# Kernel optimization log

Hardware: AMD Instinct MI355X
Metric: run time of the kernel (lower is better)

The kernel has to match this reference:

```python
import jax, jax.numpy as jnp
import numpy as np

D_MODEL = 256
N_HEADS = 8
D_HEAD = D_MODEL // N_HEADS
B = 65536
LN_EPS = 1e-5


def setup_inputs() -> dict:
    key = jax.random.key(0)
    ks = jax.random.split(key, 6)
    s = 1.0 / np.sqrt(D_MODEL)
    x = jax.random.normal(ks[0], (B, D_MODEL), dtype=jnp.float32)
    Wq = jax.random.normal(ks[1], (D_MODEL, D_MODEL), dtype=jnp.float32) * s
    Wk = jax.random.normal(ks[2], (D_MODEL, D_MODEL), dtype=jnp.float32) * s
    Wv = jax.random.normal(ks[3], (D_MODEL, D_MODEL), dtype=jnp.float32) * s
    Wout = jax.random.normal(ks[4], (D_MODEL, D_MODEL), dtype=jnp.float32) * s
    b_out = jnp.zeros((D_MODEL,), dtype=jnp.float32)
    # L initialized to identity per head (matches nn.init.eye_) plus tiny noise
    L = jnp.broadcast_to(jnp.eye(D_HEAD, dtype=jnp.float32), (N_HEADS, D_HEAD, D_HEAD)) \
        + 0.01 * jax.random.normal(ks[5], (N_HEADS, D_HEAD, D_HEAD), dtype=jnp.float32)
    gamma = jnp.ones((D_MODEL,), dtype=jnp.float32)
    beta = jnp.zeros((D_MODEL,), dtype=jnp.float32)
    return {"x": x, "Wq": Wq, "Wk": Wk, "Wv": Wv, "Wout": Wout,
            "b_out": b_out, "L": L, "gamma": gamma, "beta": beta}


def reference(x, Wq, Wk, Wv, Wout, b_out, L, gamma, beta):
    b = x.shape[0]
    # projections; view as [B, H, d_head]
    Q = (x @ Wq).reshape(b, N_HEADS, D_HEAD)
    K = (x @ Wk).reshape(b, N_HEADS, D_HEAD)
    V = (x @ Wv).reshape(b, N_HEADS, D_HEAD)
    # pairwise head differences: [B, Hq, Hk, d_head]
    diff = Q[:, :, None, :] - K[:, None, :, :]
    # per-key-head learned metric transform: L indexed by key head
    diff_t = jnp.einsum('bqkd,kdf->bqkf', diff, L)
    sq_dist = jnp.sum(diff_t * diff_t, axis=-1)            # [B, Hq, Hk]
    attn = jax.nn.softmax(-sq_dist / jnp.sqrt(jnp.float32(D_HEAD)), axis=2)
    out = jnp.einsum('bqk,bkd->bqd', attn, V).reshape(b, D_MODEL)
    out = out @ Wout + b_out
    h = out + x
    # LayerNorm over last dim
    mu = jnp.mean(h, axis=-1, keepdims=True)
    var = jnp.mean((h - mu) ** 2, axis=-1, keepdims=True)
    return (h - mu) * jax.lax.rsqrt(var + LN_EPS) * gamma + beta
```

## Files before the change

### kernel.cpp

```cpp
#include <hip/hip_runtime.h>


typedef __bf16 bf16x8 __attribute__((ext_vector_type(8)));
typedef _Float16 f16x8 __attribute__((ext_vector_type(8)));
typedef float  f32x4  __attribute__((ext_vector_type(4)));
typedef int    i32x4  __attribute__((ext_vector_type(4)));
typedef int    i32x2  __attribute__((ext_vector_type(2)));
typedef unsigned short u16;

__device__ __forceinline__ float bf2f(u16 u){
  unsigned int x = ((unsigned int)u) << 16;
  return __builtin_bit_cast(float, x);
}
__device__ __forceinline__ u16 f2bf(float f){
  unsigned int u = __builtin_bit_cast(unsigned int, f);
  u += 0x7FFFu + ((u >> 16) & 1u);
  return (u16)(u >> 16);
}
__device__ __forceinline__ unsigned int pk2(float lo, float hi){
  return ((unsigned int)f2bf(hi) << 16) | (unsigned int)f2bf(lo);
}
__device__ __forceinline__ bf16x8 ldfrag(const u16* p){
  return __builtin_bit_cast(bf16x8, *(const i32x4*)p);
}

#define LROW 264

__global__ __launch_bounds__(256) void geo_prep(
    const float* __restrict__ Wq, const float* __restrict__ Wk,
    const float* __restrict__ Wv, const float* __restrict__ Wout,
    const float* __restrict__ L, u16* __restrict__ ws)
{
  u16* Wd    = ws;
  u16* WvT   = ws + 524288;
  u16* WoutT = ws + 589824;
  const int b = blockIdx.x, t = threadIdx.x;

  if (b < 64){
    const int q = b >> 3, k = b & 7;
    __shared__ float dwb[256][33];
    __shared__ float Lk[32][33];
    for (int i = 0; i < 4; ++i){
      int idx = t + i*256;
      Lk[idx >> 5][idx & 31] = L[k*1024 + idx];
    }
    {
      const int c = t;
      const float* wqp = Wq + c*256 + q*32;
      const float* wkp = Wk + c*256 + k*32;
      #pragma unroll
      for (int j = 0; j < 8; ++j){
        f32x4 a  = *(const f32x4*)(wqp + j*4);
        f32x4 bb = *(const f32x4*)(wkp + j*4);
        #pragma unroll
        for (int p = 0; p < 4; ++p) dwb[c][j*4 + p] = a[p] - bb[p];
      }
    }
    __syncthreads();
    const int c = t;
    float wreg[32];
    #pragma unroll
    for (int d = 0; d < 32; ++d) wreg[d] = dwb[c][d];
    for (int f = 0; f < 32; ++f){
      float s = 0.f;
      #pragma unroll
      for (int d = 0; d < 32; ++d) s = fmaf(wreg[d], Lk[d][f], s);
      Wd[(size_t)(q*256 + k*32 + f)*256 + c] = f2bf(s);
    }
  } else {
    const int bb  = b - 64;
    const float* src = (bb < 16) ? Wv  : Wout;
    u16*         dst = (bb < 16) ? WvT : WoutT;
    const int tile = bb & 15;
    const int tr = tile >> 2, tc = tile & 3;
    __shared__ float tlf[64][68];
    {
      const int row = t >> 2, cs = (t & 3)*16;
      #pragma unroll
      for (int j = 0; j < 4; ++j){
        f32x4 v = *(const f32x4*)(src + (size_t)(tr*64 + row)*256 + tc*64 + cs + j*4);
        #pragma unroll
        for (int p = 0; p < 4; ++p) tlf[row][cs + j*4 + p] = v[p];
      }
    }
    __syncthreads();
    {
      const int n = t >> 2, cs = (t & 3)*16;
      float us[16];
      #pragma unroll
      for (int j = 0; j < 16; ++j) us[j] = tlf[cs + j][n];
      #pragma unroll
      for (int h = 0; h < 2; ++h){
        i32x4 o;
        #pragma unroll
        for (int p = 0; p < 4; ++p)
          o[p] = (int)pk2(us[h*8 + 2*p], us[h*8 + 2*p + 1]);
        *(i32x4*)(dst + (size_t)(tc*64 + n)*256 + tr*64 + cs + h*8) = o;
      }
    }
  }
}

__global__ __launch_bounds__(512, 4) void geo_fused(
    const float* __restrict__ x,   const u16* __restrict__ Wd,
    const u16* __restrict__ WvT,   const u16* __restrict__ WoutT,
    const float* __restrict__ b_out, const float* __restrict__ gamma,
    const float* __restrict__ beta,  float* __restrict__ out)
{
  __shared__ __align__(16) char pool[75776];
  u16  (*xs)[LROW] = (u16 (*)[LROW])(pool);
  u16  (*Vs)[LROW] = (u16 (*)[LROW])(pool + 33792);
  u16  (*ao)[LROW] = (u16 (*)[LROW])(pool);
  u16  (*hs)[256]  = (u16 (*)[256])(pool + 33792);
  _Float16* sqh    = (_Float16*)(pool + 67584);

  const int t    = threadIdx.x;
  const int lane = t & 63;
  const int w    = t >> 6;
  const int l15  = lane & 15;
  const int quad = lane >> 4;
  const long rowbase = (long)blockIdx.x * 64;

  {
    const int r  = t >> 3;
    const int c0 = (t & 7) * 32;
    const float* src = x + (rowbase + r)*256 + c0;
    unsigned int words[16];
    #pragma unroll
    for (int j = 0; j < 8; ++j){
      f32x4 v = *(const f32x4*)(src + j*4);
      words[j*2    ] = pk2(v[0], v[1]);
      words[j*2 + 1] = pk2(v[2], v[3]);
    }
    #pragma unroll
    for (int qd = 0; qd < 4; ++qd){
      i32x4 o;
      #pragma unroll
      for (int p = 0; p < 4; ++p) o[p] = (int)words[qd*4 + p];
      *(i32x4*)&xs[r][c0 + qd*8] = o;
    }
  }
  __syncthreads();

  {
    f32x4 acc[4][2];
    #pragma unroll
    for (int mt = 0; mt < 4; ++mt)
      #pragma unroll
      for (int nt = 0; nt < 2; ++nt) acc[mt][nt] = f32x4{0.f,0.f,0.f,0.f};
    #pragma unroll
    for (int kk = 0; kk < 8; ++kk){
      const int c0 = kk*32 + quad*8;
      bf16x8 a[4], bfr[2];
      #pragma unroll
      for (int mt = 0; mt < 4; ++mt) a[mt] = ldfrag(&xs[mt*16 + l15][c0]);
      #pragma unroll
      for (int nt = 0; nt < 2; ++nt){
        const int n = w*32 + nt*16 + l15;
        bfr[nt] = __builtin_bit_cast(bf16x8, *(const i32x4*)(WvT + (size_t)n*256 + c0));
      }
      #pragma unroll
      for (int mt = 0; mt < 4; ++mt)
        #pragma unroll
        for (int nt = 0; nt < 2; ++nt)
          acc[mt][nt] = __builtin_amdgcn_mfma_f32_16x16x32_bf16(a[mt], bfr[nt], acc[mt][nt], 0, 0, 0);
    }
    #pragma unroll
    for (int mt = 0; mt < 4; ++mt)
      #pragma unroll
      for (int nt = 0; nt < 2; ++nt){
        const int col = w*32 + nt*16 + l15;
        #pragma unroll
        for (int reg = 0; reg < 4; ++reg)
          Vs[mt*16 + quad*4 + reg][col] = f2bf(acc[mt][nt][reg]);
      }
  }

  {
    #pragma unroll
    for (int kp = 0; kp < 4; ++kp){
      f32x4 acc[2][2][4];
      #pragma unroll
      for (int k2 = 0; k2 < 2; ++k2)
        #pragma unroll
        for (int mt = 0; mt < 2; ++mt)
          #pragma unroll
          for (int nt = 0; nt < 4; ++nt) acc[k2][mt][nt] = f32x4{0.f,0.f,0.f,0.f};
      #pragma unroll
      for (int kk = 0; kk < 8; ++kk){
        const int c0 = kk*32 + quad*8;
        bf16x8 bfr[4];
        #pragma unroll
        for (int nt = 0; nt < 4; ++nt) bfr[nt] = ldfrag(&xs[nt*16 + l15][c0]);
        bf16x8 a[2][2];
        #pragma unroll
        for (int k2 = 0; k2 < 2; ++k2)
          #pragma unroll
          for (int mt = 0; mt < 2; ++mt){
            const int m = w*256 + (kp*2 + k2)*32 + mt*16 + l15;
            a[k2][mt] = __builtin_bit_cast(bf16x8, *(const i32x4*)(Wd + (size_t)m*256 + c0));
          }
        #pragma unroll
        for (int k2 = 0; k2 < 2; ++k2)
          #pragma unroll
          for (int mt = 0; mt < 2; ++mt)
            #pragma unroll
            for (int nt = 0; nt < 4; ++nt)
              acc[k2][mt][nt] = __builtin_amdgcn_mfma_f32_16x16x32_bf16(a[k2][mt], bfr[nt], acc[k2][mt][nt], 0, 0, 0);
      }
      #pragma unroll
      for (int k2 = 0; k2 < 2; ++k2){
        const int k = kp*2 + k2;
        #pragma unroll
        for (int nt = 0; nt < 4; ++nt){
          float s = 0.f;
          #pragma unroll
          for (int mt = 0; mt < 2; ++mt)
            #pragma unroll
            for (int reg = 0; reg < 4; ++reg){
              float d = acc[k2][mt][nt][reg];
              s = fmaf(d, d, s);
            }
          s += __shfl_xor(s, 16);
          s += __shfl_xor(s, 32);
          if (quad == 0)
            sqh[w*512 + (nt*16 + l15)*8 + k] =
                (_Float16)(s * -0.17677669529663687f);
        }
      }
    }
  }
  __syncthreads();

  {
    #pragma unroll
    for (int nt = 0; nt < 4; ++nt){
      const int r = nt*16 + l15;
      f16x8 lgh = __builtin_bit_cast(f16x8, *(const i32x4*)&sqh[w*512 + r*8]);
      float lg[8];
      #pragma unroll
      for (int k = 0; k < 8; ++k) lg[k] = (float)lgh[k];
      float mx = lg[0];
      #pragma unroll
      for (int k = 1; k < 8; ++k) mx = fmaxf(mx, lg[k]);
      float e[8], sum = 0.f;
      #pragma unroll
      for (int k = 0; k < 8; ++k){ e[k] = __expf(lg[k] - mx); sum += e[k]; }
      const float inv = 1.0f / sum;
      float o[8] = {0.f,0.f,0.f,0.f,0.f,0.f,0.f,0.f};
      #pragma unroll
      for (int k = 0; k < 8; ++k){
        i32x4 v = *(const i32x4*)&Vs[r][k*32 + quad*8];
        const float a = e[k] * inv;
        #pragma unroll
        for (int p = 0; p < 4; ++p){
          unsigned int u = (unsigned int)v[p];
          o[2*p    ] = fmaf(a, __builtin_bit_cast(float, u << 16),          o[2*p    ]);
          o[2*p + 1] = fmaf(a, __builtin_bit_cast(float, u & 0xFFFF0000u),  o[2*p + 1]);
        }
      }
      i32x4 pkv;
      #pragma unroll
      for (int p = 0; p < 4; ++p) pkv[p] = (int)pk2(o[2*p], o[2*p + 1]);
      *(i32x4*)&ao[r][w*32 + quad*8] = pkv;
    }
  }
  __syncthreads();

  {
    f32x4 acc[4][2];
    #pragma unroll
    for (int mt = 0; mt < 4; ++mt)
      #pragma unroll
      for (int nt = 0; nt < 2; ++nt) acc[mt][nt] = f32x4{0.f,0.f,0.f,0.f};
    #pragma unroll
    for (int kk = 0; kk < 8; ++kk){
      const int c0 = kk*32 + quad*8;
      bf16x8 a[4], bfr[2];
      #pragma unroll
      for (int mt = 0; mt < 4; ++mt) a[mt] = ldfrag(&ao[mt*16 + l15][c0]);
      #pragma unroll
      for (int nt = 0; nt < 2; ++nt){
        const int n = w*32 + nt*16 + l15;
        bfr[nt] = __builtin_bit_cast(bf16x8, *(const i32x4*)(WoutT + (size_t)n*256 + c0));
      }
      #pragma unroll
      for (int mt = 0; mt < 4; ++mt)
        #pragma unroll
        for (int nt = 0; nt < 2; ++nt)
          acc[mt][nt] = __builtin_amdgcn_mfma_f32_16x16x32_bf16(a[mt], bfr[nt], acc[mt][nt], 0, 0, 0);
    }
    #pragma unroll
    for (int nt = 0; nt < 2; ++nt){
      const int col = w*32 + nt*16 + l15;
      const float bo = b_out[col];
      #pragma unroll
      for (int mt = 0; mt < 4; ++mt)
        #pragma unroll
        for (int reg = 0; reg < 4; ++reg){
          const int row = mt*16 + quad*4 + reg;
          hs[row][col] = f2bf(acc[mt][nt][reg] + bo);
        }
    }
  }
  __syncthreads();

  {
    #pragma unroll
    for (int rr = 0; rr < 8; ++rr){
      const int r = w*8 + rr;
      const int c = lane*4;
      i32x2 hv2 = *(const i32x2*)&hs[r][c];
      f32x4 xv  = *(const f32x4*)(x + (rowbase + r)*256 + c);
      unsigned int u0 = (unsigned int)hv2[0], u1 = (unsigned int)hv2[1];
      f32x4 hv;
      hv[0] = __builtin_bit_cast(float, u0 << 16)         + xv[0];
      hv[1] = __builtin_bit_cast(float, u0 & 0xFFFF0000u) + xv[1];
      hv[2] = __builtin_bit_cast(float, u1 << 16)         + xv[2];
      hv[3] = __builtin_bit_cast(float, u1 & 0xFFFF0000u) + xv[3];
      float s  = hv[0] + hv[1] + hv[2] + hv[3];
      float s2 = hv[0]*hv[0] + hv[1]*hv[1] + hv[2]*hv[2] + hv[3]*hv[3];
      #pragma unroll
      for (int off = 1; off < 64; off <<= 1){
        s  += __shfl_xor(s,  off);
        s2 += __shfl_xor(s2, off);
      }
      const float mu  = s  * (1.0f/256.0f);
      const float var = s2 * (1.0f/256.0f) - mu*mu;
      const float rs  = rsqrtf(var + 1e-5f);
      f32x4 gv = *(const f32x4*)(gamma + c);
      f32x4 bv = *(const f32x4*)(beta  + c);
      f32x4 y;
      y[0] = (hv[0] - mu)*rs*gv[0] + bv[0];
      y[1] = (hv[1] - mu)*rs*gv[1] + bv[1];
      y[2] = (hv[2] - mu)*rs*gv[2] + bv[2];
      y[3] = (hv[3] - mu)*rs*gv[3] + bv[3];
      *(f32x4*)(out + (rowbase + r)*256 + c) = y;
    }
  }
}

extern "C" void kernel_launch(void* const* d_in, const int* in_sizes, int n_in,
                              void* d_out, int out_size, void* d_ws, size_t ws_size,
                              hipStream_t stream)
{
  const float* x     = (const float*)d_in[0];
  const float* Wq    = (const float*)d_in[1];
  const float* Wk    = (const float*)d_in[2];
  const float* Wv    = (const float*)d_in[3];
  const float* Wout  = (const float*)d_in[4];
  const float* b_out = (const float*)d_in[5];
  const float* L     = (const float*)d_in[6];
  const float* gamma = (const float*)d_in[7];
  const float* beta  = (const float*)d_in[8];
  u16* ws = (u16*)d_ws;

  geo_prep<<<96, 256, 0, stream>>>(Wq, Wk, Wv, Wout, L, ws);
  geo_fused<<<1024, 512, 0, stream>>>(x, ws, ws + 524288, ws + 589824,
                                      b_out, gamma, beta, (float*)d_out);
}
```

Measured before the change: 307.3 us.

## Compute Q,K,V projections then apply per-head L via MFMA instead of pairwise Wd GEMM

Replaces the precomputed 2048x256 pairwise-difference weight (Wq-Wk)·L with separate Q/K/V projections. L is then applied with small per-head MFMAs to K once and to Q for each key head, and squared distances are formed as (QL - KL). This cuts the projection work from a 2048-wide GEMM to three 256-wide GEMMs. Rows per block are halved to 32, the grid is doubled, and LDS use shrinks. Forming differences after bf16 rounding of QL and KL may lose precision compared with projecting the difference directly.

```diff
diff --git a/kernel.cpp b/kernel.cpp
--- a/kernel.cpp
+++ b/kernel.cpp
@@ -2,7 +2,6 @@
 
 
 typedef __bf16 bf16x8 __attribute__((ext_vector_type(8)));
-typedef _Float16 f16x8 __attribute__((ext_vector_type(8)));
 typedef float  f32x4  __attribute__((ext_vector_type(4)));
 typedef int    i32x4  __attribute__((ext_vector_type(4)));
 typedef int    i32x2  __attribute__((ext_vector_type(2)));
@@ -20,7 +19,10 @@
 __device__ __forceinline__ unsigned int pk2(float lo, float hi){
   return ((unsigned int)f2bf(hi) << 16) | (unsigned int)f2bf(lo);
 }
-__device__ __forceinline__ bf16x8 ldfrag(const u16* p){
+__device__ __forceinline__ bf16x8 ldfrag_lds(const u16* p){
+  return __builtin_bit_cast(bf16x8, *(const i32x4*)p);
+}
+__device__ __forceinline__ bf16x8 ldfrag_g(const u16* p){
   return __builtin_bit_cast(bf16x8, *(const i32x4*)p);
 }
 
@@ -31,47 +33,12 @@
     const float* __restrict__ Wv, const float* __restrict__ Wout,
     const float* __restrict__ L, u16* __restrict__ ws)
 {
-  u16* Wd    = ws;
-  u16* WvT   = ws + 524288;
-  u16* WoutT = ws + 589824;
   const int b = blockIdx.x, t = threadIdx.x;
-
   if (b < 64){
-    const int q = b >> 3, k = b & 7;
-    __shared__ float dwb[256][33];
-    __shared__ float Lk[32][33];
-    for (int i = 0; i < 4; ++i){
-      int idx = t + i*256;
-      Lk[idx >> 5][idx & 31] = L[k*1024 + idx];
-    }
-    {
-      const int c = t;
-      const float* wqp = Wq + c*256 + q*32;
-      const float* wkp = Wk + c*256 + k*32;
-      #pragma unroll
-      for (int j = 0; j < 8; ++j){
-        f32x4 a  = *(const f32x4*)(wqp + j*4);
-        f32x4 bb = *(const f32x4*)(wkp + j*4);
-        #pragma unroll
-        for (int p = 0; p < 4; ++p) dwb[c][j*4 + p] = a[p] - bb[p];
-      }
-    }
-    __syncthreads();
-    const int c = t;
-    float wreg[32];
-    #pragma unroll
-    for (int d = 0; d < 32; ++d) wreg[d] = dwb[c][d];
-    for (int f = 0; f < 32; ++f){
-      float s = 0.f;
-      #pragma unroll
-      for (int d = 0; d < 32; ++d) s = fmaf(wreg[d], Lk[d][f], s);
-      Wd[(size_t)(q*256 + k*32 + f)*256 + c] = f2bf(s);
-    }
-  } else {
-    const int bb  = b - 64;
-    const float* src = (bb < 16) ? Wv  : Wout;
-    u16*         dst = (bb < 16) ? WvT : WoutT;
-    const int tile = bb & 15;
+    const int m = b >> 4;
+    const float* src = (m == 0) ? Wq : (m == 1) ? Wk : (m == 2) ? Wv : Wout;
+    u16* dstbase = (m < 3) ? (ws + m*65536) : (ws + 196608);
+    const int tile = b & 15;
     const int tr = tile >> 2, tc = tile & 3;
     __shared__ float tlf[64][68];
     {
@@ -95,224 +62,238 @@
         #pragma unroll
         for (int p = 0; p < 4; ++p)
           o[p] = (int)pk2(us[h*8 + 2*p], us[h*8 + 2*p + 1]);
-        *(i32x4*)(dst + (size_t)(tc*64 + n)*256 + tr*64 + cs + h*8) = o;
-      }
-    }
+        *(i32x4*)(dstbase + (size_t)(tc*64 + n)*256 + tr*64 + cs + h*8) = o;
+      }
+    }
+  } else {
+    u16* Lt = ws + 262144;
+    const int k = t >> 5, f = t & 31;
+    for (int d = 0; d < 32; ++d)
+      Lt[k*1024 + f*32 + d] = f2bf(L[k*1024 + d*32 + f]);
   }
 }
 
 __global__ __launch_bounds__(512, 4) void geo_fused(
-    const float* __restrict__ x,   const u16* __restrict__ Wd,
-    const u16* __restrict__ WvT,   const u16* __restrict__ WoutT,
+    const float* __restrict__ x,     const u16* __restrict__ WqkvT,
+    const u16* __restrict__ WoutT,   const u16* __restrict__ Lt,
     const float* __restrict__ b_out, const float* __restrict__ gamma,
     const float* __restrict__ beta,  float* __restrict__ out)
 {
-  __shared__ __align__(16) char pool[75776];
-  u16  (*xs)[LROW] = (u16 (*)[LROW])(pool);
-  u16  (*Vs)[LROW] = (u16 (*)[LROW])(pool + 33792);
-  u16  (*ao)[LROW] = (u16 (*)[LROW])(pool);
-  u16  (*hs)[256]  = (u16 (*)[256])(pool + 33792);
-  _Float16* sqh    = (_Float16*)(pool + 67584);
+  __shared__ __align__(16) char pool[67584];
+  u16* xsU  = (u16*)(pool);
+  u16* KtsU = (u16*)(pool);
+  u16* QsU  = (u16*)(pool + 16896);
+  u16* hsU  = (u16*)(pool + 16896);
+  u16* KsU  = (u16*)(pool + 33792);
+  u16* aoU  = (u16*)(pool + 33792);
+  u16* VsU  = (u16*)(pool + 50688);
 
   const int t    = threadIdx.x;
   const int lane = t & 63;
   const int w    = t >> 6;
   const int l15  = lane & 15;
   const int quad = lane >> 4;
-  const long rowbase = (long)blockIdx.x * 64;
-
-  {
-    const int r  = t >> 3;
-    const int c0 = (t & 7) * 32;
+  const long rowbase = (long)blockIdx.x * 32;
+
+  {
+    const int r  = t >> 4;
+    const int c0 = (t & 15) * 16;
     const float* src = x + (rowbase + r)*256 + c0;
-    unsigned int words[16];
-    #pragma unroll
-    for (int j = 0; j < 8; ++j){
+    unsigned int wds[8];
+    #pragma unroll
+    for (int j = 0; j < 4; ++j){
       f32x4 v = *(const f32x4*)(src + j*4);
-      words[j*2    ] = pk2(v[0], v[1]);
-      words[j*2 + 1] = pk2(v[2], v[3]);
-    }
-    #pragma unroll
-    for (int qd = 0; qd < 4; ++qd){
+      wds[j*2    ] = pk2(v[0], v[1]);
+      wds[j*2 + 1] = pk2(v[2], v[3]);
+    }
+    #pragma unroll
+    for (int h = 0; h < 2; ++h){
       i32x4 o;
       #pragma unroll
-      for (int p = 0; p < 4; ++p) o[p] = (int)words[qd*4 + p];
-      *(i32x4*)&xs[r][c0 + qd*8] = o;
-    }
-  }
-  __syncthreads();
-
-  {
-    f32x4 acc[4][2];
-    #pragma unroll
-    for (int mt = 0; mt < 4; ++mt)
+      for (int p = 0; p < 4; ++p) o[p] = (int)wds[h*4 + p];
+      *(i32x4*)&xsU[r*LROW + c0 + h*8] = o;
+    }
+  }
+  __syncthreads();
+
+  #pragma unroll
+  for (int s = 0; s < 3; ++s){
+    const u16* Bbase = WqkvT + (size_t)(s*256 + w*32)*256;
+    u16* dst = (s == 0) ? QsU : (s == 1) ? KsU : VsU;
+    f32x4 acc[2][2];
+    #pragma unroll
+    for (int mt = 0; mt < 2; ++mt)
       #pragma unroll
       for (int nt = 0; nt < 2; ++nt) acc[mt][nt] = f32x4{0.f,0.f,0.f,0.f};
     #pragma unroll
     for (int kk = 0; kk < 8; ++kk){
       const int c0 = kk*32 + quad*8;
-      bf16x8 a[4], bfr[2];
-      #pragma unroll
-      for (int mt = 0; mt < 4; ++mt) a[mt] = ldfrag(&xs[mt*16 + l15][c0]);
-      #pragma unroll
-      for (int nt = 0; nt < 2; ++nt){
-        const int n = w*32 + nt*16 + l15;
-        bfr[nt] = __builtin_bit_cast(bf16x8, *(const i32x4*)(WvT + (size_t)n*256 + c0));
-      }
-      #pragma unroll
-      for (int mt = 0; mt < 4; ++mt)
+      bf16x8 a[2], bb[2];
+      #pragma unroll
+      for (int mt = 0; mt < 2; ++mt) a[mt] = ldfrag_lds(&xsU[(mt*16 + l15)*LROW + c0]);
+      #pragma unroll
+      for (int nt = 0; nt < 2; ++nt) bb[nt] = ldfrag_g(Bbase + (size_t)(nt*16 + l15)*256 + c0);
+      #pragma unroll
+      for (int mt = 0; mt < 2; ++mt)
         #pragma unroll
         for (int nt = 0; nt < 2; ++nt)
-          acc[mt][nt] = __builtin_amdgcn_mfma_f32_16x16x32_bf16(a[mt], bfr[nt], acc[mt][nt], 0, 0, 0);
-    }
-    #pragma unroll
-    for (int mt = 0; mt < 4; ++mt)
+          acc[mt][nt] = __builtin_amdgcn_mfma_f32_16x16x32_bf16(a[mt], bb[nt], acc[mt][nt], 0, 0, 0);
+    }
+    #pragma unroll
+    for (int mt = 0; mt < 2; ++mt)
       #pragma unroll
       for (int nt = 0; nt < 2; ++nt){
         const int col = w*32 + nt*16 + l15;
         #pragma unroll
         for (int reg = 0; reg < 4; ++reg)
-          Vs[mt*16 + quad*4 + reg][col] = f2bf(acc[mt][nt][reg]);
-      }
-  }
-
-  {
-    #pragma unroll
-    for (int kp = 0; kp < 4; ++kp){
-      f32x4 acc[2][2][4];
-      #pragma unroll
-      for (int k2 = 0; k2 < 2; ++k2)
-        #pragma unroll
-        for (int mt = 0; mt < 2; ++mt)
-          #pragma unroll
-          for (int nt = 0; nt < 4; ++nt) acc[k2][mt][nt] = f32x4{0.f,0.f,0.f,0.f};
-      #pragma unroll
-      for (int kk = 0; kk < 8; ++kk){
-        const int c0 = kk*32 + quad*8;
-        bf16x8 bfr[4];
-        #pragma unroll
-        for (int nt = 0; nt < 4; ++nt) bfr[nt] = ldfrag(&xs[nt*16 + l15][c0]);
-        bf16x8 a[2][2];
-        #pragma unroll
-        for (int k2 = 0; k2 < 2; ++k2)
-          #pragma unroll
-          for (int mt = 0; mt < 2; ++mt){
-            const int m = w*256 + (kp*2 + k2)*32 + mt*16 + l15;
-            a[k2][mt] = __builtin_bit_cast(bf16x8, *(const i32x4*)(Wd + (size_t)m*256 + c0));
-          }
-        #pragma unroll
-        for (int k2 = 0; k2 < 2; ++k2)
-          #pragma unroll
-          for (int mt = 0; mt < 2; ++mt)
-            #pragma unroll
-            for (int nt = 0; nt < 4; ++nt)
-              acc[k2][mt][nt] = __builtin_amdgcn_mfma_f32_16x16x32_bf16(a[k2][mt], bfr[nt], acc[k2][mt][nt], 0, 0, 0);
-      }
-      #pragma unroll
-      for (int k2 = 0; k2 < 2; ++k2){
-        const int k = kp*2 + k2;
-        #pragma unroll
-        for (int nt = 0; nt < 4; ++nt){
-          float s = 0.f;
-          #pragma unroll
-          for (int mt = 0; mt < 2; ++mt)
-            #pragma unroll
-            for (int reg = 0; reg < 4; ++reg){
-              float d = acc[k2][mt][nt][reg];
-              s = fmaf(d, d, s);
-            }
-          s += __shfl_xor(s, 16);
-          s += __shfl_xor(s, 32);
-          if (quad == 0)
-            sqh[w*512 + (nt*16 + l15)*8 + k] =
-                (_Float16)(s * -0.17677669529663687f);
+          dst[(mt*16 + quad*4 + reg)*LROW + col] = f2bf(acc[mt][nt][reg]);
+      }
+  }
+  __syncthreads();
+
+  {
+    bf16x8 aL[2], bK[2];
+    #pragma unroll
+    for (int mt = 0; mt < 2; ++mt)
+      aL[mt] = ldfrag_g(Lt + w*1024 + (mt*16 + l15)*32 + quad*8);
+    #pragma unroll
+    for (int nt = 0; nt < 2; ++nt)
+      bK[nt] = ldfrag_lds(&KsU[(nt*16 + l15)*LROW + w*32 + quad*8]);
+    f32x4 acc[2][2];
+    #pragma unroll
+    for (int mt = 0; mt < 2; ++mt)
+      #pragma unroll
+      for (int nt = 0; nt < 2; ++nt)
+        acc[mt][nt] = __builtin_amdgcn_mfma_f32_16x16x32_bf16(aL[mt], bK[nt],
+                        f32x4{0.f,0.f,0.f,0.f}, 0, 0, 0);
+    #pragma unroll
+    for (int mt = 0; mt < 2; ++mt)
+      #pragma unroll
+      for (int nt = 0; nt < 2; ++nt){
+        i32x2 o;
+        o[0] = (int)pk2(acc[mt][nt][0], acc[mt][nt][1]);
+        o[1] = (int)pk2(acc[mt][nt][2], acc[mt][nt][3]);
+        *(i32x2*)&KtsU[w*1024 + (nt*16 + l15)*32 + mt*16 + quad*4] = o;
+      }
+  }
+  __syncthreads();
+
+  float lg[2][8];
+  {
+    bf16x8 bQ[2];
+    #pragma unroll
+    for (int nt = 0; nt < 2; ++nt)
+      bQ[nt] = ldfrag_lds(&QsU[(nt*16 + l15)*LROW + w*32 + quad*8]);
+    #pragma unroll
+    for (int k = 0; k < 8; ++k){
+      bf16x8 aL[2];
+      #pragma unroll
+      for (int mt = 0; mt < 2; ++mt)
+        aL[mt] = ldfrag_g(Lt + k*1024 + (mt*16 + l15)*32 + quad*8);
+      f32x4 acc[2][2];
+      #pragma unroll
+      for (int mt = 0; mt < 2; ++mt)
+        #pragma unroll
+        for (int nt = 0; nt < 2; ++nt)
+          acc[mt][nt] = __builtin_amdgcn_mfma_f32_16x16x32_bf16(aL[mt], bQ[nt],
+                          f32x4{0.f,0.f,0.f,0.f}, 0, 0, 0);
+      #pragma unroll
+      for (int nt = 0; nt < 2; ++nt){
+        float s = 0.f;
+        #pragma unroll
+        for (int mt = 0; mt < 2; ++mt){
+          i32x2 kt2 = *(const i32x2*)&KtsU[k*1024 + (nt*16 + l15)*32 + mt*16 + quad*4];
+          unsigned int u0 = (unsigned int)kt2[0], u1 = (unsigned int)kt2[1];
+          float kv0 = __builtin_bit_cast(float, u0 << 16);
+          float kv1 = __builtin_bit_cast(float, u0 & 0xFFFF0000u);
+          float kv2 = __builtin_bit_cast(float, u1 << 16);
+          float kv3 = __builtin_bit_cast(float, u1 & 0xFFFF0000u);
+          float d0 = acc[mt][nt][0] - kv0, d1 = acc[mt][nt][1] - kv1;
+          float d2 = acc[mt][nt][2] - kv2, d3 = acc[mt][nt][3] - kv3;
+          s = fmaf(d0, d0, s); s = fmaf(d1, d1, s);
+          s = fmaf(d2, d2, s); s = fmaf(d3, d3, s);
         }
-      }
-    }
-  }
-  __syncthreads();
-
-  {
-    #pragma unroll
-    for (int nt = 0; nt < 4; ++nt){
+        s += __shfl_xor(s, 16);
+        s += __shfl_xor(s, 32);
+        lg[nt][k] = s * -0.17677669529663687f;
+      }
+    }
+  }
+  __syncthreads();
+
+  {
+    #pragma unroll
+    for (int nt = 0; nt < 2; ++nt){
       const int r = nt*16 + l15;
-      f16x8 lgh = __builtin_bit_cast(f16x8, *(const i32x4*)&sqh[w*512 + r*8]);
-      float lg[8];
-      #pragma unroll
-      for (int k = 0; k < 8; ++k) lg[k] = (float)lgh[k];
-      float mx = lg[0];
-      #pragma unroll
-      for (int k = 1; k < 8; ++k) mx = fmaxf(mx, lg[k]);
+      float mx = lg[nt][0];
+      #pragma unroll
+      for (int k = 1; k < 8; ++k) mx = fmaxf(mx, lg[nt][k]);
       float e[8], sum = 0.f;
       #pragma unroll
-      for (int k = 0; k < 8; ++k){ e[k] = __expf(lg[k] - mx); sum += e[k]; }
+      for (int k = 0; k < 8; ++k){ e[k] = __expf(lg[nt][k] - mx); sum += e[k]; }
       const float inv = 1.0f / sum;
       float o[8] = {0.f,0.f,0.f,0.f,0.f,0.f,0.f,0.f};
       #pragma unroll
       for (int k = 0; k < 8; ++k){
-        i32x4 v = *(const i32x4*)&Vs[r][k*32 + quad*8];
+        i32x4 v = *(const i32x4*)&VsU[r*LROW + k*32 + quad*8];
         const float a = e[k] * inv;
         #pragma unroll
         for (int p = 0; p < 4; ++p){
           unsigned int u = (unsigned int)v[p];
-          o[2*p    ] = fmaf(a, __builtin_bit_cast(float, u << 16),          o[2*p    ]);
-          o[2*p + 1] = fmaf(a, __builtin_bit_cast(float, u & 0xFFFF0000u),  o[2*p + 1]);
+          o[2*p    ] = fmaf(a, __builtin_bit_cast(float, u << 16),         o[2*p    ]);
+          o[2*p + 1] = fmaf(a, __builtin_bit_cast(float, u & 0xFFFF0000u), o[2*p + 1]);
         }
       }
       i32x4 pkv;
       #pragma unroll
       for (int p = 0; p < 4; ++p) pkv[p] = (int)pk2(o[2*p], o[2*p + 1]);
-      *(i32x4*)&ao[r][w*32 + quad*8] = pkv;
-    }
-  }
-  __syncthreads();
-
-  {
-    f32x4 acc[4][2];
-    #pragma unroll
-    for (int mt = 0; mt < 4; ++mt)
+      *(i32x4*)&aoU[r*LROW + w*32 + quad*8] = pkv;
+    }
+  }
+  __syncthreads();
+
+  {
+    f32x4 acc[2][2];
+    #pragma unroll
+    for (int mt = 0; mt < 2; ++mt)
       #pragma unroll
       for (int nt = 0; nt < 2; ++nt) acc[mt][nt] = f32x4{0.f,0.f,0.f,0.f};
     #pragma unroll
     for (int kk = 0; kk < 8; ++kk){
       const int c0 = kk*32 + quad*8;
-      bf16x8 a[4], bfr[2];
-      #pragma unroll
-      for (int mt = 0; mt < 4; ++mt) a[mt] = ldfrag(&ao[mt*16 + l15][c0]);
-      #pragma unroll
-      for (int nt = 0; nt < 2; ++nt){
-        const int n = w*32 + nt*16 + l15;
-        bfr[nt] = __builtin_bit_cast(bf16x8, *(const i32x4*)(WoutT + (size_t)n*256 + c0));
-      }
-      #pragma unroll
-      for (int mt = 0; mt < 4; ++mt)
+      bf16x8 a[2], bb[2];
+      #pragma unroll
+      for (int mt = 0; mt < 2; ++mt) a[mt] = ldfrag_lds(&aoU[(mt*16 + l15)*LROW + c0]);
+      #pragma unroll
+      for (int nt = 0; nt < 2; ++nt)
+        bb[nt] = ldfrag_g(WoutT + (size_t)(w*32 + nt*16 + l15)*256 + c0);
+      #pragma unroll
+      for (int mt = 0; mt < 2; ++mt)
         #pragma unroll
         for (int nt = 0; nt < 2; ++nt)
-          acc[mt][nt] = __builtin_amdgcn_mfma_f32_16x16x32_bf16(a[mt], bfr[nt], acc[mt][nt], 0, 0, 0);
+          acc[mt][nt] = __builtin_amdgcn_mfma_f32_16x16x32_bf16(a[mt], bb[nt], acc[mt][nt], 0, 0, 0);
     }
     #pragma unroll
     for (int nt = 0; nt < 2; ++nt){
       const int col = w*32 + nt*16 + l15;
       const float bo = b_out[col];
       #pragma unroll
-      for (int mt = 0; mt < 4; ++mt)
-        #pragma unroll
-        for (int reg = 0; reg < 4; ++reg){
-          const int row = mt*16 + quad*4 + reg;
-          hs[row][col] = f2bf(acc[mt][nt][reg] + bo);
-        }
-    }
-  }
-  __syncthreads();
-
-  {
-    #pragma unroll
-    for (int rr = 0; rr < 8; ++rr){
-      const int r = w*8 + rr;
+      for (int mt = 0; mt < 2; ++mt)
+        #pragma unroll
+        for (int reg = 0; reg < 4; ++reg)
+          hsU[(mt*16 + quad*4 + reg)*256 + col] = f2bf(acc[mt][nt][reg] + bo);
+    }
+  }
+  __syncthreads();
+
+  {
+    #pragma unroll
+    for (int rr = 0; rr < 4; ++rr){
+      const int r = w*4 + rr;
       const int c = lane*4;
-      i32x2 hv2 = *(const i32x2*)&hs[r][c];
-      f32x4 xv  = *(const f32x4*)(x + (rowbase + r)*256 + c);
-      unsigned int u0 = (unsigned int)hv2[0], u1 = (unsigned int)hv2[1];
+      i32x2 h2 = *(const i32x2*)&hsU[r*256 + c];
+      f32x4 xv = *(const f32x4*)(x + (rowbase + r)*256 + c);
+      unsigned int u0 = (unsigned int)h2[0], u1 = (unsigned int)h2[1];
       f32x4 hv;
       hv[0] = __builtin_bit_cast(float, u0 << 16)         + xv[0];
       hv[1] = __builtin_bit_cast(float, u0 & 0xFFFF0000u) + xv[1];
@@ -355,7 +336,7 @@
   const float* beta  = (const float*)d_in[8];
   u16* ws = (u16*)d_ws;
 
-  geo_prep<<<96, 256, 0, stream>>>(Wq, Wk, Wv, Wout, L, ws);
-  geo_fused<<<1024, 512, 0, stream>>>(x, ws, ws + 524288, ws + 589824,
+  geo_prep<<<65, 256, 0, stream>>>(Wq, Wk, Wv, Wout, L, ws);
+  geo_fused<<<2048, 512, 0, stream>>>(x, ws, ws + 196608, ws + 262144,
                                       b_out, gamma, beta, (float*)d_out);
 }
```

Measured after the change: 266.9 us. 1.15x faster.
